# Kernel tuning notes

Measured on AMD Instinct MI355X. Metric: run time of the kernel, lower is better.

The kernel has to match this reference:

```python
import jax, jax.numpy as jnp
import numpy as np

NUM_HEADS = 16
NUM_KV_HEADS = 4
HEAD_DIM = 64
HIDDEN = 1024
B, S = 2, 2048


def setup_inputs() -> dict:
    key = jax.random.key(0)
    ks = jax.random.split(key, 9)
    sc = 0.02
    return {
        "x": jax.random.normal(ks[0], (B, S, HIDDEN), dtype=jnp.float32),
        "Wq": jax.random.normal(ks[1], (HIDDEN, NUM_HEADS * HEAD_DIM), dtype=jnp.float32) * sc,
        "bq": jnp.zeros((NUM_HEADS * HEAD_DIM,), dtype=jnp.float32),
        "Wk": jax.random.normal(ks[2], (HIDDEN, NUM_KV_HEADS * HEAD_DIM), dtype=jnp.float32) * sc,
        "bk": jnp.zeros((NUM_KV_HEADS * HEAD_DIM,), dtype=jnp.float32),
        "Wv": jax.random.normal(ks[3], (HIDDEN, NUM_KV_HEADS * HEAD_DIM), dtype=jnp.float32) * sc,
        "bv": jnp.zeros((NUM_KV_HEADS * HEAD_DIM,), dtype=jnp.float32),
        "Wo": jax.random.normal(ks[4], (NUM_HEADS * HEAD_DIM, HIDDEN), dtype=jnp.float32) * sc,
        "bo": jnp.zeros((HIDDEN,), dtype=jnp.float32),
    }


def reference(x, Wq, bq, Wk, bk, Wv, bv, Wo, bo):
    bs, seq, _ = x.shape
    groups = NUM_HEADS // NUM_KV_HEADS
    # projections -> [B, H, S, D]
    q = (x @ Wq + bq).reshape(bs, seq, NUM_HEADS, HEAD_DIM).transpose(0, 2, 1, 3)
    k = (x @ Wk + bk).reshape(bs, seq, NUM_KV_HEADS, HEAD_DIM).transpose(0, 2, 1, 3)
    v = (x @ Wv + bv).reshape(bs, seq, NUM_KV_HEADS, HEAD_DIM).transpose(0, 2, 1, 3)
    # repeat_interleave KV heads to match query heads (GQA expansion)
    k = jnp.repeat(k, groups, axis=1)
    v = jnp.repeat(v, groups, axis=1)
    # NOTE: source applies NO 1/sqrt(d) scaling and no mask/ALiBi
    scores = jnp.einsum("bhqd,bhkd->bhqk", q, k)
    attn = jax.nn.softmax(scores.astype(jnp.float32), axis=-1).astype(q.dtype)
    out = jnp.einsum("bhqk,bhkd->bhqd", attn, v)
    out = out.transpose(0, 2, 1, 3).reshape(bs, seq, NUM_HEADS * HEAD_DIM)
    return out @ Wo + bo
```

## Files before the change

kernel.cpp:

```cpp
#include <hip/hip_runtime.h>

#define NHEADS 16
#define NKV    4
#define HDIM   64
#define HIDDEN 1024
#define BATCH  2
#define SEQ    2048
#define MROWS  (BATCH * SEQ)
#define LOG2E  1.44269504088896340736f

typedef __bf16 bf16_t;
typedef bf16_t bf16x8 __attribute__((ext_vector_type(8)));
typedef float  f32x4  __attribute__((ext_vector_type(4)));

__device__ __forceinline__ float bf2f(unsigned short u) {
    return __uint_as_float(((unsigned int)u) << 16);
}
__device__ __forceinline__ unsigned short f2bf(float f) {
    unsigned int u = __float_as_uint(f);
    u += 0x7FFFu + ((u >> 16) & 1u);
    return (unsigned short)(u >> 16);
}

__device__ __forceinline__ void gld16(const unsigned short* g, unsigned short* l)
{
    __builtin_amdgcn_global_load_lds(
        (const __attribute__((address_space(1))) void*)g,
        (__attribute__((address_space(3))) void*)l,
        16, 0, 0);
}

__device__ __forceinline__ int swz(int row, int ch) {
    return (row * 8 + (ch ^ (row & 7))) * 8;
}
__device__ __forceinline__ int swz16(int row, int ch) {
    return (row * 16 + (ch ^ (row & 7))) * 8;
}

__device__ __forceinline__ bool sniff_is_f32(const unsigned short* __restrict__ x)
{
    const int e = (x[threadIdx.x & 63] >> 7) & 0xFF;
    const unsigned long long ok = __ballot(e >= 110 && e <= 140);
    return __popcll(ok) < 56;
}

__device__ __forceinline__ void load8cvt(const void* base, size_t elem, bool isf32, unsigned short out[8])
{
    if (!isf32) {
        *(uint4*)out = *(const uint4*)((const unsigned short*)base + elem);
    } else {
        const float* p = (const float*)base + elem;
        float4 v0 = *(const float4*)p;
        float4 v1 = *(const float4*)(p + 4);
        out[0] = f2bf(v0.x); out[1] = f2bf(v0.y); out[2] = f2bf(v0.z); out[3] = f2bf(v0.w);
        out[4] = f2bf(v1.x); out[5] = f2bf(v1.y); out[6] = f2bf(v1.z); out[7] = f2bf(v1.w);
    }
}
__device__ __forceinline__ float bias_at(const void* b, int i, bool isf32)
{
    return isf32 ? ((const float*)b)[i] : bf2f(((const unsigned short*)b)[i]);
}

__global__ __launch_bounds__(256)
void prep_kernel(const void* __restrict__ x,
                 const void* __restrict__ Wq, const void* __restrict__ Wk,
                 const void* __restrict__ Wv, const void* __restrict__ Wo,
                 unsigned short* __restrict__ xb,
                 unsigned short* __restrict__ Wqkvt,
                 unsigned short* __restrict__ Wot)
{
    const bool isf32 = sniff_is_f32((const unsigned short*)x);
    const int t = threadIdx.x;
    int bid = blockIdx.x;

    if (bid < 2048) {
        if (!isf32) return;
        const size_t c = (size_t)bid * 256 + t;
        unsigned short v[8];
        load8cvt(x, c * 8, true, v);
        *(uint4*)(&xb[c * 8]) = *(uint4*)v;
        return;
    }
    bid -= 2048;
    const void* src; unsigned short* dst; int N, rowoff;
    if (bid < 256)      {             src = Wq; dst = Wqkvt; N = 1024; rowoff = 0;    }
    else if (bid < 320) { bid -= 256; src = Wk; dst = Wqkvt; N = 256;  rowoff = 1024; }
    else if (bid < 384) { bid -= 320; src = Wv; dst = Wqkvt; N = 256;  rowoff = 1280; }
    else                { bid -= 384; src = Wo; dst = Wot;   N = 1024; rowoff = 0;    }
    const int ntx = N / 64;
    const int gn0 = (bid % ntx) * 64;
    const int gk0 = (bid / ntx) * 64;

    __shared__ unsigned short Ts[64][72];
#pragma unroll
    for (int half = 0; half < 2; ++half) {
        const int kl = (t >> 3) + half * 32;
        const int n8 = (t & 7) * 8;
        unsigned short v[8];
        load8cvt(src, (size_t)(gk0 + kl) * N + gn0 + n8, isf32, v);
        *(uint4*)(&Ts[kl][n8]) = *(uint4*)v;
    }
    __syncthreads();
#pragma unroll
    for (int half = 0; half < 2; ++half) {
        const int nl = (t >> 3) + half * 32;
        const int k8 = (t & 7) * 8;
        unsigned short v[8];
#pragma unroll
        for (int j = 0; j < 8; ++j) v[j] = Ts[k8 + j][nl];
        *(uint4*)(&dst[(size_t)(rowoff + gn0 + nl) * HIDDEN + gk0 + k8]) = *(uint4*)v;
    }
}

template<int TBM, int TBN>
__device__ __forceinline__ void gemm_tile(const unsigned short* __restrict__ A,
                                          const unsigned short* __restrict__ Bt,
                                          int K, int m0, int n0,
                                          unsigned short* As, unsigned short* Bs,
                                          f32x4 (&acc)[TBM / 32][TBN / 32])
{
    const int tid  = threadIdx.x;
    const int lane = tid & 63;
    const int wave = tid >> 6;
    const int quad = lane >> 4;
    const int l15  = lane & 15;
    const int wr   = wave >> 1;
    const int wc   = wave & 1;

    for (int k0 = 0; k0 < K; k0 += 128) {
#pragma unroll
        for (int r = 0; r < TBM / 16; ++r) {
            const int u = r * 256 + tid;
            const int row = u >> 4;
            const int gch = ((u & 15) ^ (row & 7)) * 8;
            gld16(&A[(size_t)(m0 + row) * K + k0 + gch], &As[(r * 256 + wave * 64) * 8]);
        }
#pragma unroll
        for (int r = 0; r < TBN / 16; ++r) {
            const int u = r * 256 + tid;
            const int row = u >> 4;
            const int gch = ((u & 15) ^ (row & 7)) * 8;
            gld16(&Bt[(size_t)(n0 + row) * K + k0 + gch], &Bs[(r * 256 + wave * 64) * 8]);
        }
        __syncthreads();

#pragma unroll
        for (int kk = 0; kk < 4; ++kk) {
            bf16x8 af[TBM / 32], bfv[TBN / 32];
#pragma unroll
            for (int i = 0; i < TBM / 32; ++i)
                af[i] = *(const bf16x8*)(&As[swz16(wr * (TBM / 2) + i * 16 + l15, kk * 4 + quad)]);
#pragma unroll
            for (int j = 0; j < TBN / 32; ++j)
                bfv[j] = *(const bf16x8*)(&Bs[swz16(wc * (TBN / 2) + j * 16 + l15, kk * 4 + quad)]);
#pragma unroll
            for (int i = 0; i < TBM / 32; ++i)
#pragma unroll
                for (int j = 0; j < TBN / 32; ++j)
                    acc[i][j] = __builtin_amdgcn_mfma_f32_16x16x32_bf16(af[i], bfv[j], acc[i][j], 0, 0, 0);
        }
        __syncthreads();
    }
}

__global__ __launch_bounds__(256)
void gemm_qkv(const void* __restrict__ xraw,
              const unsigned short* __restrict__ xb,
              const unsigned short* __restrict__ Bt,
              const void* __restrict__ bq, const void* __restrict__ bk,
              const void* __restrict__ bv,
              unsigned short* __restrict__ Qh,
              unsigned short* __restrict__ Kh,
              unsigned short* __restrict__ Vt)
{
    __shared__ __align__(16) unsigned short As[64 * 128];
    __shared__ __align__(16) unsigned short Bs[64 * 128];
    const bool bias_f32 = sniff_is_f32((const unsigned short*)xraw);
    const unsigned short* A = bias_f32 ? xb : (const unsigned short*)xraw;
    const int lane = threadIdx.x & 63;
    const int wave = threadIdx.x >> 6;
    const int quad = lane >> 4, l15 = lane & 15;
    const int wr = wave >> 1, wc = wave & 1;
    const int m0 = blockIdx.y * 64, n0 = blockIdx.x * 64;

    f32x4 acc[2][2] = {};
    gemm_tile<64, 64>(A, Bt, HIDDEN, m0, n0, As, Bs, acc);

#pragma unroll
    for (int i = 0; i < 2; ++i) {
#pragma unroll
        for (int j = 0; j < 2; ++j) {
            const int nn  = n0 + wc * 32 + j * 16 + l15;
            const int mmb = m0 + wr * 32 + i * 16 + quad * 4;
            const int b = mmb >> 11, s0 = mmb & 2047;
            if (nn < 1024) {
                const float bias = bias_at(bq, nn, bias_f32);
                const int h = nn >> 6, d = nn & 63;
                const size_t idx0 = (((size_t)(b * NHEADS + h)) * SEQ + s0) * 64 + d;
#pragma unroll
                for (int r = 0; r < 4; ++r)
                    Qh[idx0 + (size_t)r * 64] = f2bf((acc[i][j][r] + bias) * LOG2E);
            } else if (nn < 1280) {
                const int nk = nn - 1024;
                const float bias = bias_at(bk, nk, bias_f32);
                const int h = nk >> 6, d = nk & 63;
                const size_t idx0 = (((size_t)(b * NKV + h)) * SEQ + s0) * 64 + d;
#pragma unroll
                for (int r = 0; r < 4; ++r)
                    Kh[idx0 + (size_t)r * 64] = f2bf(acc[i][j][r] + bias);
            } else {
                const int nv = nn - 1280;
                const float bias = bias_at(bv, nv, bias_f32);
                const int h = nv >> 6, d = nv & 63;
                const size_t idx = (((size_t)(b * NKV + h)) * 64 + d) * SEQ + s0;
                unsigned short vv[4];
#pragma unroll
                for (int r = 0; r < 4; ++r) vv[r] = f2bf(acc[i][j][r] + bias);
                *(uint2*)(&Vt[idx]) = *(uint2*)vv;
            }
        }
    }
}

__global__ __launch_bounds__(256)
void gemm_o(const void* __restrict__ xraw,
            const unsigned short* __restrict__ A,
            const unsigned short* __restrict__ Bt,
            const void* __restrict__ bo,
            float* __restrict__ out)
{
    __shared__ __align__(16) unsigned short As[64 * 128];
    __shared__ __align__(16) unsigned short Bs[64 * 128];
    const bool bias_f32 = sniff_is_f32((const unsigned short*)xraw);
    const int lane = threadIdx.x & 63;
    const int wave = threadIdx.x >> 6;
    const int quad = lane >> 4, l15 = lane & 15;
    const int wr = wave >> 1, wc = wave & 1;
    const int m0 = blockIdx.y * 64, n0 = blockIdx.x * 64;

    f32x4 acc[2][2] = {};
    gemm_tile<64, 64>(A, Bt, HIDDEN, m0, n0, As, Bs, acc);

#pragma unroll
    for (int i = 0; i < 2; ++i) {
#pragma unroll
        for (int j = 0; j < 2; ++j) {
            const int nn = n0 + wc * 32 + j * 16 + l15;
            const float bvv = bias_at(bo, nn, bias_f32);
#pragma unroll
            for (int r = 0; r < 4; ++r) {
                const int mm = m0 + wr * 32 + i * 16 + quad * 4 + r;
                out[(size_t)mm * HIDDEN + nn] = acc[i][j][r] + bvv;
            }
        }
    }
}

#define PLD 68
__global__ __launch_bounds__(256)
void attn_kernel(const unsigned short* __restrict__ Qh,
                 const unsigned short* __restrict__ Kh,
                 const unsigned short* __restrict__ Vt,
                 unsigned short* __restrict__ O)
{
    __shared__ __align__(16) unsigned short Kth[64 * 64];
    __shared__ __align__(16) unsigned short VtT[64 * 64];
    __shared__ __align__(16) unsigned short Pt[4][16 * PLD];

    const int tid  = threadIdx.x;
    const int lane = tid & 63;
    const int wave = tid >> 6;
    const int quad = lane >> 4;
    const int l15  = lane & 15;

    const int qt = blockIdx.x;
    const int h  = blockIdx.y;
    const int b  = blockIdx.z;
    const int kv = h >> 2;

    const size_t qoff = ((size_t)(b * NHEADS + h)) * SEQ * HDIM;
    const size_t koff = ((size_t)(b * NKV + kv)) * SEQ * HDIM;
    const size_t voff = ((size_t)(b * NKV + kv)) * HDIM * SEQ;

    const int q0 = qt * 64 + wave * 16;

    const size_t qrow = qoff + (size_t)(q0 + l15) * HDIM;
    const bf16x8 qh0 = *(const bf16x8*)(&Qh[qrow + quad * 8]);
    const bf16x8 qh1 = *(const bf16x8*)(&Qh[qrow + 32 + quad * 8]);

    f32x4 o[4] = {};
    float lsum = 0.0f;

    const int srow0 = tid >> 3;
    const int schp  = tid & 7;

    const unsigned short* Khs = Kh + koff;
    const unsigned short* Vts = Vt + voff;

    for (int kt = 0; kt < SEQ / 64; ++kt, Khs += 64 * HDIM, Vts += 64) {
#pragma unroll
        for (int c = 0; c < 2; ++c) {
            const int row = srow0 + c * 32;
            const int gch = (schp ^ (row & 7)) * 8;
            gld16(&Khs[(size_t)row * 64 + gch],  &Kth[(c * 256 + wave * 64) * 8]);
            gld16(&Vts[(size_t)row * SEQ + gch], &VtT[(c * 256 + wave * 64) * 8]);
        }
        __syncthreads();

        f32x4 s[4];
#pragma unroll
        for (int j = 0; j < 4; ++j) {
            const int rr = j * 16 + l15;
            bf16x8 kh0 = *(const bf16x8*)(&Kth[swz(rr, quad)]);
            bf16x8 kh1 = *(const bf16x8*)(&Kth[swz(rr, quad ^ 4)]);
            f32x4 z = {};
            z = __builtin_amdgcn_mfma_f32_16x16x32_bf16(kh0, qh0, z, 0, 0, 0);
            s[j] = __builtin_amdgcn_mfma_f32_16x16x32_bf16(kh1, qh1, z, 0, 0, 0);
        }

#pragma unroll
        for (int j = 0; j < 4; ++j) {
            const float p0 = __builtin_amdgcn_exp2f(s[j][0]);
            const float p1 = __builtin_amdgcn_exp2f(s[j][1]);
            const float p2 = __builtin_amdgcn_exp2f(s[j][2]);
            const float p3 = __builtin_amdgcn_exp2f(s[j][3]);
            lsum += (p0 + p1) + (p2 + p3);
            uint2 w;
            w.x = __builtin_amdgcn_perm(__float_as_uint(p1), __float_as_uint(p0), 0x07060302u);
            w.y = __builtin_amdgcn_perm(__float_as_uint(p3), __float_as_uint(p2), 0x07060302u);
            *(uint2*)(&Pt[wave][l15 * PLD + j * 16 + quad * 4]) = w;
        }

#pragma unroll
        for (int kk = 0; kk < 2; ++kk) {
            bf16x8 pf = *(const bf16x8*)(&Pt[wave][l15 * PLD + kk * 32 + quad * 8]);
#pragma unroll
            for (int dt = 0; dt < 4; ++dt) {
                bf16x8 vf = *(const bf16x8*)(&VtT[swz(dt * 16 + l15, kk * 4 + quad)]);
                o[dt] = __builtin_amdgcn_mfma_f32_16x16x32_bf16(vf, pf, o[dt], 0, 0, 0);
            }
        }
        __syncthreads();
    }

    lsum += __shfl_xor(lsum, 16);
    lsum += __shfl_xor(lsum, 32);

    const float inv = 1.0f / lsum;
    const size_t rowbase = ((size_t)b * SEQ + (q0 + l15)) * (NHEADS * HDIM) + h * HDIM;
#pragma unroll
    for (int dt = 0; dt < 4; ++dt) {
        unsigned short v4[4];
#pragma unroll
        for (int r = 0; r < 4; ++r) v4[r] = f2bf(o[dt][r] * inv);
        *(uint2*)(&O[rowbase + dt * 16 + quad * 4]) = *(uint2*)v4;
    }
}

extern "C" void kernel_launch(void* const* d_in, const int* in_sizes, int n_in,
                              void* d_out, int out_size, void* d_ws, size_t ws_size,
                              hipStream_t stream)
{
    const void* x  = d_in[0];
    const void* Wq = d_in[1];
    const void* bq = d_in[2];
    const void* Wk = d_in[3];
    const void* bk = d_in[4];
    const void* Wv = d_in[5];
    const void* bv = d_in[6];
    const void* Wo = d_in[7];
    const void* bo = d_in[8];
    float* out = (float*)d_out;

    unsigned short* p = (unsigned short*)d_ws;
    unsigned short* xb    = p; p += (size_t)MROWS * HIDDEN;
    unsigned short* Wqkvt = p; p += (size_t)1536 * HIDDEN;
    unsigned short* Wot   = p; p += (size_t)HIDDEN * HIDDEN;
    unsigned short* Qh = p;  p += (size_t)MROWS * 1024;
    unsigned short* Kh = p;  p += (size_t)2 * NKV * SEQ * HDIM;
    unsigned short* Vt = p;  p += (size_t)2 * NKV * SEQ * HDIM;
    unsigned short* A2 = p;  p += (size_t)MROWS * 1024;

    dim3 blk(256);
    prep_kernel<<<dim3(2688), blk, 0, stream>>>(x, Wq, Wk, Wv, Wo, xb, Wqkvt, Wot);
    gemm_qkv<<<dim3(1536 / 64, MROWS / 64), blk, 0, stream>>>(
        x, xb, Wqkvt, bq, bk, bv, Qh, Kh, Vt);
    attn_kernel<<<dim3(SEQ / 64, NHEADS, BATCH), blk, 0, stream>>>(Qh, Kh, Vt, A2);
    gemm_o<<<dim3(1024 / 64, MROWS / 64), blk, 0, stream>>>(x, A2, Wot, bo, out);
}
```

Baseline: 186.5 us.

## Process two 16-row query tiles per wave in attention, halving block size

The attention kernel now runs 2 waves per block instead of 4, and each wave handles 32 query rows as two 16-row sub-tiles. K fragments and V fragments read from LDS are reused across both sub-tiles, which halves LDS read traffic per MFMA. The cooperative K/V tile load is spread over 4 iterations per thread instead of 2. The cost is more registers per thread for the doubled accumulators, and fewer waves per block to hide latency.

New measurement: 187.0 us. Within noise of the previous version (+0.3%).

```diff
diff --git a/kernel.cpp b/kernel.cpp
--- a/kernel.cpp
+++ b/kernel.cpp
@@ -257,7 +257,7 @@
 }
 
 #define PLD 68
-__global__ __launch_bounds__(256)
+__global__ __launch_bounds__(128)
 void attn_kernel(const unsigned short* __restrict__ Qh,
                  const unsigned short* __restrict__ Kh,
                  const unsigned short* __restrict__ Vt,
@@ -265,7 +265,7 @@
 {
     __shared__ __align__(16) unsigned short Kth[64 * 64];
     __shared__ __align__(16) unsigned short VtT[64 * 64];
-    __shared__ __align__(16) unsigned short Pt[4][16 * PLD];
+    __shared__ __align__(16) unsigned short Pt[2][2][16 * PLD];
 
     const int tid  = threadIdx.x;
     const int lane = tid & 63;
@@ -282,78 +282,100 @@
     const size_t koff = ((size_t)(b * NKV + kv)) * SEQ * HDIM;
     const size_t voff = ((size_t)(b * NKV + kv)) * HDIM * SEQ;
 
-    const int q0 = qt * 64 + wave * 16;
-
-    const size_t qrow = qoff + (size_t)(q0 + l15) * HDIM;
-    const bf16x8 qh0 = *(const bf16x8*)(&Qh[qrow + quad * 8]);
-    const bf16x8 qh1 = *(const bf16x8*)(&Qh[qrow + 32 + quad * 8]);
-
-    f32x4 o[4] = {};
-    float lsum = 0.0f;
-
-    const int srow0 = tid >> 3;
-    const int schp  = tid & 7;
+    const int q0 = qt * 64 + wave * 32;
+
+    const size_t qrA = qoff + (size_t)(q0 + l15) * HDIM;
+    const size_t qrB = qoff + (size_t)(q0 + 16 + l15) * HDIM;
+    const bf16x8 qA0 = *(const bf16x8*)(&Qh[qrA + quad * 8]);
+    const bf16x8 qA1 = *(const bf16x8*)(&Qh[qrA + 32 + quad * 8]);
+    const bf16x8 qB0 = *(const bf16x8*)(&Qh[qrB + quad * 8]);
+    const bf16x8 qB1 = *(const bf16x8*)(&Qh[qrB + 32 + quad * 8]);
+
+    f32x4 oA[4] = {}, oB[4] = {};
+    float lsA = 0.0f, lsB = 0.0f;
 
     const unsigned short* Khs = Kh + koff;
     const unsigned short* Vts = Vt + voff;
 
     for (int kt = 0; kt < SEQ / 64; ++kt, Khs += 64 * HDIM, Vts += 64) {
 #pragma unroll
-        for (int c = 0; c < 2; ++c) {
-            const int row = srow0 + c * 32;
-            const int gch = (schp ^ (row & 7)) * 8;
-            gld16(&Khs[(size_t)row * 64 + gch],  &Kth[(c * 256 + wave * 64) * 8]);
-            gld16(&Vts[(size_t)row * SEQ + gch], &VtT[(c * 256 + wave * 64) * 8]);
+        for (int c = 0; c < 4; ++c) {
+            const int u = c * 128 + tid;
+            const int row = u >> 3;
+            const int gch = ((u & 7) ^ (row & 7)) * 8;
+            gld16(&Khs[(size_t)row * 64 + gch],  &Kth[(c * 128 + wave * 64) * 8]);
+            gld16(&Vts[(size_t)row * SEQ + gch], &VtT[(c * 128 + wave * 64) * 8]);
         }
         __syncthreads();
 
-        f32x4 s[4];
+        f32x4 sA[4], sB[4];
 #pragma unroll
         for (int j = 0; j < 4; ++j) {
             const int rr = j * 16 + l15;
             bf16x8 kh0 = *(const bf16x8*)(&Kth[swz(rr, quad)]);
             bf16x8 kh1 = *(const bf16x8*)(&Kth[swz(rr, quad ^ 4)]);
-            f32x4 z = {};
-            z = __builtin_amdgcn_mfma_f32_16x16x32_bf16(kh0, qh0, z, 0, 0, 0);
-            s[j] = __builtin_amdgcn_mfma_f32_16x16x32_bf16(kh1, qh1, z, 0, 0, 0);
+            f32x4 zA = {};
+            zA = __builtin_amdgcn_mfma_f32_16x16x32_bf16(kh0, qA0, zA, 0, 0, 0);
+            sA[j] = __builtin_amdgcn_mfma_f32_16x16x32_bf16(kh1, qA1, zA, 0, 0, 0);
+            f32x4 zB = {};
+            zB = __builtin_amdgcn_mfma_f32_16x16x32_bf16(kh0, qB0, zB, 0, 0, 0);
+            sB[j] = __builtin_amdgcn_mfma_f32_16x16x32_bf16(kh1, qB1, zB, 0, 0, 0);
         }
 
 #pragma unroll
         for (int j = 0; j < 4; ++j) {
-            const float p0 = __builtin_amdgcn_exp2f(s[j][0]);
-            const float p1 = __builtin_amdgcn_exp2f(s[j][1]);
-            const float p2 = __builtin_amdgcn_exp2f(s[j][2]);
-            const float p3 = __builtin_amdgcn_exp2f(s[j][3]);
-            lsum += (p0 + p1) + (p2 + p3);
-            uint2 w;
-            w.x = __builtin_amdgcn_perm(__float_as_uint(p1), __float_as_uint(p0), 0x07060302u);
-            w.y = __builtin_amdgcn_perm(__float_as_uint(p3), __float_as_uint(p2), 0x07060302u);
-            *(uint2*)(&Pt[wave][l15 * PLD + j * 16 + quad * 4]) = w;
+            const float a0 = __builtin_amdgcn_exp2f(sA[j][0]);
+            const float a1 = __builtin_amdgcn_exp2f(sA[j][1]);
+            const float a2 = __builtin_amdgcn_exp2f(sA[j][2]);
+            const float a3 = __builtin_amdgcn_exp2f(sA[j][3]);
+            lsA += (a0 + a1) + (a2 + a3);
+            uint2 wA;
+            wA.x = __builtin_amdgcn_perm(__float_as_uint(a1), __float_as_uint(a0), 0x07060302u);
+            wA.y = __builtin_amdgcn_perm(__float_as_uint(a3), __float_as_uint(a2), 0x07060302u);
+            *(uint2*)(&Pt[wave][0][l15 * PLD + j * 16 + quad * 4]) = wA;
+
+            const float b0 = __builtin_amdgcn_exp2f(sB[j][0]);
+            const float b1 = __builtin_amdgcn_exp2f(sB[j][1]);
+            const float b2 = __builtin_amdgcn_exp2f(sB[j][2]);
+            const float b3 = __builtin_amdgcn_exp2f(sB[j][3]);
+            lsB += (b0 + b1) + (b2 + b3);
+            uint2 wB;
+            wB.x = __builtin_amdgcn_perm(__float_as_uint(b1), __float_as_uint(b0), 0x07060302u);
+            wB.y = __builtin_amdgcn_perm(__float_as_uint(b3), __float_as_uint(b2), 0x07060302u);
+            *(uint2*)(&Pt[wave][1][l15 * PLD + j * 16 + quad * 4]) = wB;
         }
 
 #pragma unroll
         for (int kk = 0; kk < 2; ++kk) {
-            bf16x8 pf = *(const bf16x8*)(&Pt[wave][l15 * PLD + kk * 32 + quad * 8]);
+            bf16x8 pfA = *(const bf16x8*)(&Pt[wave][0][l15 * PLD + kk * 32 + quad * 8]);
+            bf16x8 pfB = *(const bf16x8*)(&Pt[wave][1][l15 * PLD + kk * 32 + quad * 8]);
 #pragma unroll
             for (int dt = 0; dt < 4; ++dt) {
                 bf16x8 vf = *(const bf16x8*)(&VtT[swz(dt * 16 + l15, kk * 4 + quad)]);
-                o[dt] = __builtin_amdgcn_mfma_f32_16x16x32_bf16(vf, pf, o[dt], 0, 0, 0);
+                oA[dt] = __builtin_amdgcn_mfma_f32_16x16x32_bf16(vf, pfA, oA[dt], 0, 0, 0);
+                oB[dt] = __builtin_amdgcn_mfma_f32_16x16x32_bf16(vf, pfB, oB[dt], 0, 0, 0);
             }
         }
         __syncthreads();
     }
 
-    lsum += __shfl_xor(lsum, 16);
-    lsum += __shfl_xor(lsum, 32);
-
-    const float inv = 1.0f / lsum;
-    const size_t rowbase = ((size_t)b * SEQ + (q0 + l15)) * (NHEADS * HDIM) + h * HDIM;
+    lsA += __shfl_xor(lsA, 16);  lsA += __shfl_xor(lsA, 32);
+    lsB += __shfl_xor(lsB, 16);  lsB += __shfl_xor(lsB, 32);
+
+    const float invA = 1.0f / lsA;
+    const float invB = 1.0f / lsB;
+    const size_t rbA = ((size_t)b * SEQ + (q0 + l15)) * (NHEADS * HDIM) + h * HDIM;
+    const size_t rbB = ((size_t)b * SEQ + (q0 + 16 + l15)) * (NHEADS * HDIM) + h * HDIM;
 #pragma unroll
     for (int dt = 0; dt < 4; ++dt) {
-        unsigned short v4[4];
-#pragma unroll
-        for (int r = 0; r < 4; ++r) v4[r] = f2bf(o[dt][r] * inv);
-        *(uint2*)(&O[rowbase + dt * 16 + quad * 4]) = *(uint2*)v4;
+        unsigned short vA[4], vB[4];
+#pragma unroll
+        for (int r = 0; r < 4; ++r) {
+            vA[r] = f2bf(oA[dt][r] * invA);
+            vB[r] = f2bf(oB[dt][r] * invB);
+        }
+        *(uint2*)(&O[rbA + dt * 16 + quad * 4]) = *(uint2*)vA;
+        *(uint2*)(&O[rbB + dt * 16 + quad * 4]) = *(uint2*)vB;
     }
 }
 
@@ -381,10 +403,9 @@
     unsigned short* Vt = p;  p += (size_t)2 * NKV * SEQ * HDIM;
     unsigned short* A2 = p;  p += (size_t)MROWS * 1024;
 
-    dim3 blk(256);
-    prep_kernel<<<dim3(2688), blk, 0, stream>>>(x, Wq, Wk, Wv, Wo, xb, Wqkvt, Wot);
-    gemm_qkv<<<dim3(1536 / 64, MROWS / 64), blk, 0, stream>>>(
+    prep_kernel<<<dim3(2688), dim3(256), 0, stream>>>(x, Wq, Wk, Wv, Wo, xb, Wqkvt, Wot);
+    gemm_qkv<<<dim3(1536 / 64, MROWS / 64), dim3(256), 0, stream>>>(
         x, xb, Wqkvt, bq, bk, bv, Qh, Kh, Vt);
-    attn_kernel<<<dim3(SEQ / 64, NHEADS, BATCH), blk, 0, stream>>>(Qh, Kh, Vt, A2);
-    gemm_o<<<dim3(1024 / 64, MROWS / 64), blk, 0, stream>>>(x, A2, Wot, bo, out);
-}
+    attn_kernel<<<dim3(SEQ / 64, NHEADS, BATCH), dim3(128), 0, stream>>>(Qh, Kh, Vt, A2);
+    gemm_o<<<dim3(1024 / 64, MROWS / 64), dim3(256), 0, stream>>>(x, A2, Wot, bo, out);
+}
```
